# Optimization experiments

Hardware: AMD Instinct MI355X
Metric: run time of the kernel (lower is better)

Reference implementation:

```python
import jax, jax.numpy as jnp
import numpy as np

HIDDEN = 1024
HEADS = 16
HEAD_DIM = HIDDEN // HEADS


def setup_inputs() -> dict:
    key = jax.random.key(0)
    ks = jax.random.split(key, 7)
    B, S, H = 8, 1024, HIDDEN
    hidden_states = jax.random.normal(ks[0], (B, S, H), dtype=jnp.float32)
    attention_mask = jnp.zeros((B, 1, 1, S), dtype=jnp.float32)
    # Xavier-uniform weights [out, in], zero biases (matches module init)
    limit = float(np.sqrt(6.0 / (H + H)))
    Wq = jax.random.uniform(ks[1], (H, H), minval=-limit, maxval=limit, dtype=jnp.float32)
    Wk = jax.random.uniform(ks[2], (H, H), minval=-limit, maxval=limit, dtype=jnp.float32)
    Wv = jax.random.uniform(ks[3], (H, H), minval=-limit, maxval=limit, dtype=jnp.float32)
    bq = jnp.zeros((H,), dtype=jnp.float32)
    bk = jnp.zeros((H,), dtype=jnp.float32)
    bv = jnp.zeros((H,), dtype=jnp.float32)
    return {"hidden_states": hidden_states, "attention_mask": attention_mask,
            "Wq": Wq, "bq": bq, "Wk": Wk, "bk": bk, "Wv": Wv, "bv": bv}


def _split_heads(x):
    # [B, S, H] -> [B, heads, S, head_dim]
    B, S, _ = x.shape
    return x.reshape(B, S, HEADS, HEAD_DIM).transpose(0, 2, 1, 3)


def reference(hidden_states, attention_mask, Wq, bq, Wk, bk, Wv, bv):
    # Linear projections: y = x @ W^T + b  (weights stored [out, in] as in torch)
    q = _split_heads(hidden_states @ Wq.T + bq)
    k = _split_heads(hidden_states @ Wk.T + bk)
    v = _split_heads(hidden_states @ Wv.T + bv)
    scale = 1.0 / (HEAD_DIM ** 0.5)
    scores = jnp.einsum('bhqd,bhkd->bhqk', q, k) * scale  # [B,heads,S,S]
    scores = scores + attention_mask
    probs = jax.nn.softmax(scores, axis=-1)
    # dropout is identity at inference
    ctx = jnp.einsum('bhqk,bhkd->bhqd', probs, v)
    B, _, S, _ = ctx.shape
    return ctx.transpose(0, 2, 1, 3).reshape(B, S, HIDDEN)
```

## Files before the change

### kernel.cpp

```cpp
#include <hip/hip_runtime.h>
#include <hip/hip_bf16.h>
#include <stdint.h>

#define B_ 8
#define S_ 1024
#define NH_ 16
#define D_ 64
#define H_ 1024
#define M_TOT (B_*S_)
#define LOG2E 1.44269504088896f

typedef __attribute__((ext_vector_type(8))) short short8;
typedef __attribute__((ext_vector_type(4))) float f32x4;
typedef __attribute__((ext_vector_type(16))) float f32x16;

#if __has_builtin(__builtin_amdgcn_exp2f)
#define EXP2(x) __builtin_amdgcn_exp2f(x)
#else
#define EXP2(x) __expf((x) * 0.69314718056f)
#endif

static __device__ __forceinline__ unsigned short f2bf(float f) {
  union { float f; unsigned u; } c; c.f = f;
  unsigned u = c.u;
  return (unsigned short)((u + 0x7fffu + ((u >> 16) & 1u)) >> 16);
}

static __device__ __forceinline__ void gld_lds16(void* lds, const void* g) {
  __builtin_amdgcn_global_load_lds((const __attribute__((address_space(1))) unsigned*)g,
                                   (__attribute__((address_space(3))) unsigned*)lds, 16, 0, 0);
}

#define WAIT_LGKM0() asm volatile("s_waitcnt lgkmcnt(0)" ::: "memory")
#define WAIT_VM(n)   asm volatile("s_waitcnt vmcnt(" #n ")" ::: "memory")
#define SBAR()       __builtin_amdgcn_s_barrier()
#define SCHED0()     __builtin_amdgcn_sched_barrier(0)
#define PRIO1()      __builtin_amdgcn_s_setprio(1)
#define PRIO0()      __builtin_amdgcn_s_setprio(0)

__global__ void cvt_f32_bf16(const float* __restrict__ X,
                             const float* __restrict__ Wq,
                             const float* __restrict__ Wk,
                             const float* __restrict__ Wv,
                             unsigned short* __restrict__ Xbf,
                             unsigned short* __restrict__ Wbf) {
  const long long NX = (long long)M_TOT * H_;
  const long long NW = (long long)H_ * H_;
  long long t = (long long)blockIdx.x * blockDim.x + threadIdx.x;
  const long long stride = (long long)gridDim.x * blockDim.x;
  const long long total4 = (NX + 3 * NW) >> 2;
  for (; t < total4; t += stride) {
    long long e = t << 2;
    const float* src; unsigned short* dst;
    if (e < NX) { src = X + e; dst = Xbf + e; }
    else {
      long long r = e - NX;
      int w = (int)(r / NW);
      long long o = r - (long long)w * NW;
      src = (w == 0 ? Wq : (w == 1 ? Wk : Wv)) + o;
      dst = Wbf + (long long)w * NW + o;
    }
    float4 v = *(const float4*)src;
    ushort4 u;
    u.x = f2bf(v.x); u.y = f2bf(v.y); u.z = f2bf(v.z); u.w = f2bf(v.w);
    *(ushort4*)dst = u;
  }
}

#define QBM 256
#define QBN 256
#define QBK 64
#define REG_B 32768
#define BUFSZ 65536
#define VBUF  49152

#define MMQ(I0, J0, AF, BF)                                               \
  _Pragma("unroll")                                                       \
  for (int a_ = 0; a_ < 4; ++a_)                                          \
    _Pragma("unroll")                                                     \
    for (int b_ = 0; b_ < 2; ++b_)                                        \
      _Pragma("unroll")                                                   \
      for (int k_ = 0; k_ < 2; ++k_)                                      \
        acc[(I0) + a_][(J0) + b_] = __builtin_amdgcn_mfma_f32_16x16x32_bf16( \
            AF[a_][k_], BF[b_][k_], acc[(I0) + a_][(J0) + b_], 0, 0, 0);

#define RD_A(BUF, MS)                                                     \
  _Pragma("unroll")                                                       \
  for (int f_ = 0; f_ < 4; ++f_)                                          \
    _Pragma("unroll")                                                     \
    for (int k_ = 0; k_ < 2; ++k_) A[f_][k_] = rdA(BUF, MS, f_, k_);

#define RD_B(DST, BUF, NS)                                                \
  _Pragma("unroll")                                                       \
  for (int f_ = 0; f_ < 2; ++f_)                                          \
    _Pragma("unroll")                                                     \
    for (int k_ = 0; k_ < 2; ++k_) DST[f_][k_] = rdB(BUF, NS, f_, k_);

__global__ __launch_bounds__(512, 1) void qkv_gemm_qk(
    const unsigned short* __restrict__ Xbf,
    const unsigned short* __restrict__ Wbf,
    const float* __restrict__ bq, const float* __restrict__ bk,
    unsigned short* __restrict__ Qo, unsigned short* __restrict__ Ko) {
  __shared__ char lds[2 * BUFSZ];

  const int tid = threadIdx.x;
  const int w = tid >> 6;
  const int l = tid & 63;
  const int lrow = l & 15, lgrp = l >> 4;
  const int wm = w >> 2, wn = w & 3;

  const int orig = blockIdx.x;
  const int xcd = orig & 7;
  const int slot = orig >> 3;
  const int nz = slot >> 2;
  const int mtile = (xcd * 4 + (slot & 3)) * QBM;
  const int ntile = (nz & 3) * QBN;
  const int z = nz >> 2;

  const unsigned short* Wz = Wbf + (long long)z * H_ * H_;

  const int srow = l >> 3;
  const int sslot = l & 7;
  auto stageOpA = [&](char* buf, int half, int k0) {
    #pragma unroll
    for (int jj = 0; jj < 2; ++jj) {
      int j = w * 2 + jj;
      int row = half * 128 + j * 8 + srow;
      int so = (sslot ^ (row & 7)) * 8;
      gld_lds16(buf + (half * 16 + j) * 1024,
                Xbf + (long long)(mtile + row) * H_ + k0 + so);
    }
  };
  auto stageOpB = [&](char* buf, int half, int k0) {
    #pragma unroll
    for (int jj = 0; jj < 2; ++jj) {
      int j = w * 2 + jj;
      int row = half * 128 + j * 8 + srow;
      int so = (sslot ^ (row & 7)) * 8;
      gld_lds16(buf + REG_B + (half * 16 + j) * 1024,
                Wz + (long long)(ntile + row) * H_ + k0 + so);
    }
  };

  auto rdA = [&](const char* buf, int ms, int fi, int ks) -> short8 {
    int r = ms * 128 + wm * 64 + fi * 16 + lrow;
    return *(const short8*)(buf + r * 128 + (((ks * 4 + lgrp) ^ (r & 7)) * 16));
  };
  auto rdB = [&](const char* buf, int ns, int fj, int ks) -> short8 {
    int r = ns * 128 + wn * 32 + fj * 16 + lrow;
    return *(const short8*)(buf + REG_B + r * 128 + (((ks * 4 + lgrp) ^ (r & 7)) * 16));
  };

  f32x4 acc[8][4];
  f32x4 zero = {0.f, 0.f, 0.f, 0.f};
  #pragma unroll
  for (int a = 0; a < 8; ++a)
    #pragma unroll
    for (int c = 0; c < 4; ++c) acc[a][c] = zero;

  short8 A[4][2], B0[2][2], B1[2][2];

  stageOpA(lds, 0, 0);
  stageOpB(lds, 0, 0);
  stageOpB(lds, 1, 0);
  stageOpA(lds, 1, 0);
  stageOpA(lds + BUFSZ, 0, QBK);
  SCHED0(); WAIT_VM(6); SCHED0();
  SBAR();

  #pragma unroll 1
  for (int t = 0; t < 15; ++t) {
    char* bc = lds + ((t & 1) ? BUFSZ : 0);
    char* bn = lds + ((t & 1) ? 0 : BUFSZ);
    const int k1 = (t + 1) * QBK;
    const int k2 = (t + 2) * QBK;
    const bool st2 = (t + 2 < 16);

    RD_A(bc, 0);
    RD_B(B0, bc, 0);
    stageOpB(bn, 0, k1);
    WAIT_LGKM0(); SCHED0();
    PRIO1(); MMQ(0, 0, A, B0); PRIO0();
    SCHED0(); WAIT_VM(6); SCHED0();
    SBAR();

    RD_B(B1, bc, 1);
    stageOpB(bn, 1, k1);
    WAIT_LGKM0(); SCHED0();
    PRIO1(); MMQ(0, 2, A, B1); PRIO0();
    SCHED0(); WAIT_VM(6); SCHED0();
    SBAR();

    RD_A(bc, 1);
    stageOpA(bn, 1, k1);
    WAIT_LGKM0(); SCHED0();
    PRIO1(); MMQ(4, 2, A, B1); PRIO0();
    SCHED0(); WAIT_VM(6); SCHED0();
    SBAR();

    if (st2) stageOpA(bc, 0, k2);
    PRIO1(); MMQ(4, 0, A, B0); PRIO0();
    SCHED0(); WAIT_VM(6); SCHED0();
    SBAR();
  }

  SCHED0(); WAIT_VM(0); SCHED0();
  SBAR();
  {
    char* bc = lds + BUFSZ;
    RD_A(bc, 0);
    RD_B(B0, bc, 0);
    WAIT_LGKM0(); SCHED0();
    PRIO1(); MMQ(0, 0, A, B0); PRIO0();
    RD_B(B1, bc, 1);
    WAIT_LGKM0(); SCHED0();
    PRIO1(); MMQ(0, 2, A, B1); PRIO0();
    RD_A(bc, 1);
    WAIT_LGKM0(); SCHED0();
    PRIO1(); MMQ(4, 2, A, B1); MMQ(4, 0, A, B0); PRIO0();
  }

  const float* bias = (z == 0) ? bq : bk;
  unsigned short* O = (z == 0) ? Qo : Ko;
  #pragma unroll
  for (int nj = 0; nj < 4; ++nj) {
    int n = ntile + (nj >> 1) * 128 + wn * 32 + (nj & 1) * 16 + lrow;
    float bv_ = bias[n];
    int h = n >> 6, d = n & 63;
    #pragma unroll
    for (int mi = 0; mi < 8; ++mi)
      #pragma unroll
      for (int r = 0; r < 4; ++r) {
        int m = mtile + (mi >> 2) * 128 + wm * 64 + (mi & 3) * 16 + lgrp * 4 + r;
        float val = acc[mi][nj][r] + bv_;
        if (z == 0) val *= 0.125f * LOG2E;
        int b = m >> 10, s = m & 1023;
        O[(((long long)(b * NH_ + h)) * S_ + s) * D_ + d] = f2bf(val);
      }
  }
}

__global__ __launch_bounds__(512, 1) void qkv_gemm_v(
    const unsigned short* __restrict__ Xbf,
    const unsigned short* __restrict__ Wbf,
    const float* __restrict__ bv,
    unsigned short* __restrict__ Vt) {
  __shared__ char lds[3 * VBUF];

  const int tid = threadIdx.x;
  const int w = tid >> 6;
  const int l = tid & 63;
  const int lrow = l & 15, lgrp = l >> 4;
  const int wm = w >> 2, wn = w & 3;

  const int orig = blockIdx.x;
  const int xcd = orig & 7;
  const int slot = orig >> 3;
  const int mtile = (xcd * 8 + (slot & 7)) * 128;
  const int ntile = (slot >> 3) * QBN;

  const unsigned short* Wz = Wbf + 2LL * H_ * H_;

  const int srow = l >> 3;
  const int sslot = l & 7;
  auto stageW = [&](char* buf, int half, int k0) {
    #pragma unroll
    for (int jj = 0; jj < 2; ++jj) {
      int j = w * 2 + jj;
      int row = half * 128 + j * 8 + srow;
      int so = (sslot ^ (row & 7)) * 8;
      gld_lds16(buf + (half * 16 + j) * 1024,
                Wz + (long long)(ntile + row) * H_ + k0 + so);
    }
  };
  auto stageX = [&](char* buf, int k0) {
    #pragma unroll
    for (int jj = 0; jj < 2; ++jj) {
      int j = w * 2 + jj;
      int row = j * 8 + srow;
      int so = (sslot ^ (row & 7)) * 8;
      gld_lds16(buf + 32768 + j * 1024,
                Xbf + (long long)(mtile + row) * H_ + k0 + so);
    }
  };

  auto rdA = [&](const char* buf, int ms, int fi, int ks) -> short8 {
    int r = ms * 128 + wm * 64 + fi * 16 + lrow;
    return *(const short8*)(buf + r * 128 + (((ks * 4 + lgrp) ^ (r & 7)) * 16));
  };
  auto rdB = [&](const char* buf, int ns, int fj, int ks) -> short8 {
    int r = wn * 32 + fj * 16 + lrow;
    (void)ns;
    return *(const short8*)(buf + 32768 + r * 128 + (((ks * 4 + lgrp) ^ (r & 7)) * 16));
  };

  f32x4 acc[8][2];
  f32x4 zero = {0.f, 0.f, 0.f, 0.f};
  #pragma unroll
  for (int a = 0; a < 8; ++a)
    #pragma unroll
    for (int c = 0; c < 2; ++c) acc[a][c] = zero;

  short8 A[4][2], B0[2][2];

  stageW(lds, 0, 0); stageW(lds, 1, 0); stageX(lds, 0);
  stageW(lds + VBUF, 0, QBK); stageW(lds + VBUF, 1, QBK); stageX(lds + VBUF, QBK);
  SCHED0(); WAIT_VM(6); SCHED0();
  SBAR();

  #pragma unroll 1
  for (int t = 0; t < 16; ++t) {
    char* bc = lds + (t % 3) * VBUF;
    char* b2 = lds + ((t + 2) % 3) * VBUF;
    const int k2 = (t + 2) * QBK;
    const bool st2 = (t + 2 < 16);

    RD_A(bc, 0);
    RD_B(B0, bc, 0);
    if (st2) { stageW(b2, 0, k2); stageW(b2, 1, k2); }
    WAIT_LGKM0(); SCHED0();
    PRIO1(); MMQ(0, 0, A, B0); PRIO0();
    SCHED0(); WAIT_VM(6); SCHED0();
    SBAR();

    RD_A(bc, 1);
    if (st2) stageX(b2, k2);
    WAIT_LGKM0(); SCHED0();
    PRIO1(); MMQ(4, 0, A, B0); PRIO0();
    SCHED0();
    if (t < 14) { WAIT_VM(6); } else { WAIT_VM(0); }
    SCHED0();
    SBAR();
  }

  #pragma unroll
  for (int mi = 0; mi < 8; ++mi)
    #pragma unroll
    for (int r = 0; r < 4; ++r) {
      int nfull = ntile + (mi >> 2) * 128 + wm * 64 + (mi & 3) * 16 + lgrp * 4 + r;
      float bv_ = bv[nfull];
      int h = nfull >> 6, d = nfull & 63;
      #pragma unroll
      for (int nj = 0; nj < 2; ++nj) {
        int mfull = mtile + wn * 32 + nj * 16 + lrow;
        float val = acc[mi][nj][r] + bv_;
        int b = mfull >> 10, s = mfull & 1023;
        Vt[(((long long)(b * NH_ + h)) * D_ + d) * S_ + s] = f2bf(val);
      }
    }
}

__global__ __launch_bounds__(256, 2) void attn_fused(
    const unsigned short* __restrict__ Qbf,
    const unsigned short* __restrict__ Kbf,
    const unsigned short* __restrict__ Vtb,
    const float* __restrict__ mask,
    float* __restrict__ out) {
  __shared__ char lds[2 * 16384 + 4096];
  char* ldsM = lds + 32768;
  const int tid = threadIdx.x, w = tid >> 6, l = tid & 63;
  const int l31 = l & 31, h = l >> 5;

  const int lid = blockIdx.x;
  const int xcd = lid & 7, k = lid >> 3;
  const int bh = xcd * 16 + (k >> 3);
  const int qt = k & 7;
  const int b = bh >> 4, hd = bh & 15;
  const int q0 = qt * 128 + w * 32;

  const unsigned short* Kg = Kbf + (long long)bh * S_ * D_;
  const unsigned short* Vg = Vtb + (long long)bh * D_ * S_;
  const float* mrow = mask + b * S_;

  auto stageKV = [&](int kt, char* buf) {
    const int key0 = kt * 64;
    #pragma unroll
    for (int t = 0; t < 2; ++t) {
      int j = w * 2 + t;
      int row = j * 8 + (l >> 3);
      int so = ((l & 7) ^ (row & 7)) * 8;
      gld_lds16(buf + j * 1024,        Kg + (long long)(key0 + row) * D_ + so);
      gld_lds16(buf + 8192 + j * 1024, Vg + (long long)row * S_ + key0 + so);
    }
  };

  short8 qf[4];
  #pragma unroll
  for (int ks = 0; ks < 4; ++ks)
    qf[ks] = *(const short8*)(Qbf + ((long long)bh * S_ + q0 + l31) * D_ + ks * 16 + 8 * h);
  {
    float4 mv = *(const float4*)(mrow + tid * 4);
    f32x4 mt;
    mt[0] = mv.x * LOG2E - 12.f;
    mt[1] = mv.y * LOG2E - 12.f;
    mt[2] = mv.z * LOG2E - 12.f;
    mt[3] = mv.w * LOG2E - 12.f;
    *(f32x4*)(ldsM + tid * 16) = mt;
  }
  stageKV(0, lds);
  SCHED0(); WAIT_VM(0); SCHED0();
  __syncthreads();

  f32x16 acc[2];
  #pragma unroll
  for (int db = 0; db < 2; ++db)
    #pragma unroll
    for (int r = 0; r < 16; ++r) acc[db][r] = 0.f;
  float l_run = 0.f;

  #pragma unroll 1
  for (int kt = 0; kt < S_ / 64; ++kt) {
    char* ldsK = lds + (kt & 1) * 16384;
    char* ldsV = ldsK + 8192;
    const int key0 = kt * 64;
    const bool st = (kt + 1 < S_ / 64);

    if (st) stageKV(kt + 1, lds + ((kt + 1) & 1) * 16384);

    f32x16 sc[2];
    #pragma unroll
    for (int kb = 0; kb < 2; ++kb)
      #pragma unroll
      for (int r = 0; r < 16; ++r) sc[kb][r] = 0.f;

    #pragma unroll
    for (int kb = 0; kb < 2; ++kb) {
      short8 kf[4];
      #pragma unroll
      for (int ks = 0; ks < 4; ++ks) {
        int row = kb * 32 + l31;
        int g = (2 * ks + h) ^ (row & 7);
        kf[ks] = *(const short8*)(ldsK + row * 128 + g * 16);
      }
      PRIO1();
      #pragma unroll
      for (int ks = 0; ks < 4; ++ks)
        sc[kb] = __builtin_amdgcn_mfma_f32_32x32x16_bf16(
            kf[ks], qf[ks], sc[kb], 0, 0, 0);
      PRIO0();
    }

    float sv[32];
    #pragma unroll
    for (int kb = 0; kb < 2; ++kb)
      #pragma unroll
      for (int rg = 0; rg < 4; ++rg) {
        f32x4 m4 = *(const f32x4*)(ldsM + (key0 + kb * 32 + rg * 8 + 4 * h) * 4);
        #pragma unroll
        for (int c = 0; c < 4; ++c)
          sv[kb * 16 + rg * 4 + c] = EXP2(sc[kb][rg * 4 + c] + m4[c]);
      }
    {
      float r16[16];
      #pragma unroll
      for (int i = 0; i < 16; ++i) r16[i] = sv[i] + sv[i + 16];
      #pragma unroll
      for (int i = 0; i < 8; ++i) r16[i] = r16[i] + r16[i + 8];
      #pragma unroll
      for (int i = 0; i < 4; ++i) r16[i] = r16[i] + r16[i + 4];
      float ps = (r16[0] + r16[1]) + (r16[2] + r16[3]);
      float xs = ps, ys = ps;
      asm volatile("v_permlane32_swap_b32 %0, %1" : "+v"(xs), "+v"(ys));
      l_run += xs + ys;
    }

    short8 pfrag[4];
    {
      unsigned Wd[8][2];
      #pragma unroll
      for (int j = 0; j < 8; ++j) {
        int base = (j >> 2) * 16 + (j & 3) * 4;
        asm("v_cvt_pk_bf16_f32 %0, %1, %2" : "=v"(Wd[j][0]) : "v"(sv[base + 0]), "v"(sv[base + 1]));
        asm("v_cvt_pk_bf16_f32 %0, %1, %2" : "=v"(Wd[j][1]) : "v"(sv[base + 2]), "v"(sv[base + 3]));
      }
      #pragma unroll
      for (int ks = 0; ks < 4; ++ks) {
        unsigned x0 = Wd[2 * ks][0], y0 = Wd[2 * ks + 1][0];
        unsigned x1 = Wd[2 * ks][1], y1 = Wd[2 * ks + 1][1];
        asm volatile("v_permlane32_swap_b32 %0, %1" : "+v"(x0), "+v"(y0));
        asm volatile("v_permlane32_swap_b32 %0, %1" : "+v"(x1), "+v"(y1));
        union { unsigned u[4]; short8 s; } fu;
        fu.u[0] = x0;
        fu.u[1] = x1;
        fu.u[2] = y0;
        fu.u[3] = y1;
        pfrag[ks] = fu.s;
      }
    }

    #pragma unroll
    for (int db = 0; db < 2; ++db) {
      short8 vf[4];
      #pragma unroll
      for (int ks = 0; ks < 4; ++ks) {
        int row = db * 32 + l31;
        int g = (2 * ks + h) ^ (row & 7);
        vf[ks] = *(const short8*)(ldsV + row * 128 + g * 16);
      }
      PRIO1();
      #pragma unroll
      for (int ks = 0; ks < 4; ++ks)
        acc[db] = __builtin_amdgcn_mfma_f32_32x32x16_bf16(
            vf[ks], pfrag[ks], acc[db], 0, 0, 0);
      PRIO0();
    }

    if (st) { SCHED0(); WAIT_VM(0); SCHED0(); SBAR(); }
  }

  {
    float inv = 1.0f / l_run;
    int q = q0 + l31;
    float* orow = out + ((long long)b * S_ + q) * H_ + hd * D_;
    #pragma unroll
    for (int db = 0; db < 2; ++db)
      #pragma unroll
      for (int rg = 0; rg < 4; ++rg) {
        f32x4 v4;
        #pragma unroll
        for (int c = 0; c < 4; ++c) v4[c] = acc[db][rg * 4 + c] * inv;
        *(f32x4*)(orow + db * 32 + rg * 8 + 4 * h) = v4;
      }
  }
}

extern "C" void kernel_launch(void* const* d_in, const int* in_sizes, int n_in,
                              void* d_out, int out_size, void* d_ws, size_t ws_size,
                              hipStream_t stream) {
  const float* X    = (const float*)d_in[0];
  const float* mask = (const float*)d_in[1];
  const float* Wq   = (const float*)d_in[2];
  const float* bq   = (const float*)d_in[3];
  const float* Wk   = (const float*)d_in[4];
  const float* bk   = (const float*)d_in[5];
  const float* Wv   = (const float*)d_in[6];
  const float* bv   = (const float*)d_in[7];
  float* out = (float*)d_out;

  char* ws = (char*)d_ws;
  unsigned short* Xbf = (unsigned short*)ws;
  unsigned short* Wbf = (unsigned short*)(ws + 16777216);
  unsigned short* Qb  = (unsigned short*)(ws + 23068672);
  unsigned short* Kb  = (unsigned short*)(ws + 39845888);
  unsigned short* Vt  = (unsigned short*)(ws + 56623104);

  hipLaunchKernelGGL(cvt_f32_bf16, dim3(2048), dim3(256), 0, stream,
                     X, Wq, Wk, Wv, Xbf, Wbf);
  hipLaunchKernelGGL(qkv_gemm_qk, dim3(256), dim3(512), 0, stream,
                     Xbf, Wbf, bq, bk, Qb, Kb);
  hipLaunchKernelGGL(qkv_gemm_v, dim3(256), dim3(512), 0, stream,
                     Xbf, Wbf, bv, Vt);
  hipLaunchKernelGGL(attn_fused, dim3(1024), dim3(256), 0, stream,
                     Qb, Kb, Vt, mask, out);
}
```

Baseline: 117.1 us.

## Software-pipeline QK^T one tile ahead of softmax and PV in attention

Restructures the attention key loop so the QK^T MFMA for tile t+1 is issued before the exp/softmax and PV work of tile t, using ping-pong score registers (scA/scB) and a two-iteration unrolled loop. K and V staging are split: K is prefetched two tiles ahead and V one tile ahead, each with its own double buffer. The goal is to overlap matrix-core work with the exp and conversion VALU work and hide load latency. This costs extra VGPRs for the second score buffer, which could hurt occupancy at launch bounds (256,2), and relies on the barrier placement being correct for the new buffer reuse distances.

```diff
diff --git a/kernel.cpp b/kernel.cpp
--- a/kernel.cpp
+++ b/kernel.cpp
@@ -350,13 +350,108 @@
     }
 }
 
+#define ATTN_QK(DST, KBUF)                                                 \
+  {                                                                        \
+    _Pragma("unroll")                                                      \
+    for (int kb_ = 0; kb_ < 2; ++kb_) {                                    \
+      short8 kf[4];                                                        \
+      _Pragma("unroll")                                                    \
+      for (int ks_ = 0; ks_ < 4; ++ks_) {                                  \
+        int row_ = kb_ * 32 + l31;                                         \
+        int g_ = (2 * ks_ + h) ^ (row_ & 7);                               \
+        kf[ks_] = *(const short8*)((KBUF) + row_ * 128 + g_ * 16);         \
+      }                                                                    \
+      _Pragma("unroll")                                                    \
+      for (int r_ = 0; r_ < 16; ++r_) DST[kb_][r_] = 0.f;                  \
+      PRIO1();                                                             \
+      _Pragma("unroll")                                                    \
+      for (int ks_ = 0; ks_ < 4; ++ks_)                                    \
+        DST[kb_] = __builtin_amdgcn_mfma_f32_32x32x16_bf16(                \
+            kf[ks_], qf[ks_], DST[kb_], 0, 0, 0);                          \
+      PRIO0();                                                             \
+    }                                                                      \
+  }
+
+#define ATTN_BODY(T, CUR, NXT)                                             \
+  {                                                                        \
+    const int t_ = (T);                                                    \
+    const bool hasN = (t_ + 1 < 16);                                       \
+    if (t_ + 2 < 16) stageK(t_ + 2, lds + ((t_ & 1) << 13));               \
+    if (hasN) stageV(t_ + 1, lds + 16384 + (((t_ + 1) & 1) << 13));        \
+    if (hasN) { ATTN_QK(NXT, lds + (((t_ + 1) & 1) << 13)); }              \
+    const int key0_ = t_ * 64;                                             \
+    _Pragma("unroll")                                                      \
+    for (int kb_ = 0; kb_ < 2; ++kb_)                                      \
+      _Pragma("unroll")                                                    \
+      for (int rg_ = 0; rg_ < 4; ++rg_) {                                  \
+        f32x4 m4 = *(const f32x4*)(ldsM + (key0_ + kb_ * 32 + rg_ * 8 + 4 * h) * 4); \
+        _Pragma("unroll")                                                  \
+        for (int c_ = 0; c_ < 4; ++c_)                                     \
+          CUR[kb_][rg_ * 4 + c_] = EXP2(CUR[kb_][rg_ * 4 + c_] + m4[c_]);  \
+      }                                                                    \
+    {                                                                      \
+      float r16[16];                                                       \
+      _Pragma("unroll")                                                    \
+      for (int i_ = 0; i_ < 16; ++i_) r16[i_] = CUR[0][i_] + CUR[1][i_];   \
+      _Pragma("unroll")                                                    \
+      for (int i_ = 0; i_ < 8; ++i_) r16[i_] = r16[i_] + r16[i_ + 8];      \
+      _Pragma("unroll")                                                    \
+      for (int i_ = 0; i_ < 4; ++i_) r16[i_] = r16[i_] + r16[i_ + 4];      \
+      float ps = (r16[0] + r16[1]) + (r16[2] + r16[3]);                    \
+      float xs = ps, ys = ps;                                              \
+      asm volatile("v_permlane32_swap_b32 %0, %1" : "+v"(xs), "+v"(ys));   \
+      l_run += xs + ys;                                                    \
+    }                                                                      \
+    short8 pfrag[4];                                                       \
+    {                                                                      \
+      unsigned Wd[8][2];                                                   \
+      _Pragma("unroll")                                                    \
+      for (int j_ = 0; j_ < 8; ++j_) {                                     \
+        asm("v_cvt_pk_bf16_f32 %0, %1, %2" : "=v"(Wd[j_][0])               \
+            : "v"(CUR[j_ >> 2][(j_ & 3) * 4 + 0]), "v"(CUR[j_ >> 2][(j_ & 3) * 4 + 1])); \
+        asm("v_cvt_pk_bf16_f32 %0, %1, %2" : "=v"(Wd[j_][1])               \
+            : "v"(CUR[j_ >> 2][(j_ & 3) * 4 + 2]), "v"(CUR[j_ >> 2][(j_ & 3) * 4 + 3])); \
+      }                                                                    \
+      _Pragma("unroll")                                                    \
+      for (int ks_ = 0; ks_ < 4; ++ks_) {                                  \
+        unsigned x0 = Wd[2 * ks_][0], y0 = Wd[2 * ks_ + 1][0];             \
+        unsigned x1 = Wd[2 * ks_][1], y1 = Wd[2 * ks_ + 1][1];             \
+        asm volatile("v_permlane32_swap_b32 %0, %1" : "+v"(x0), "+v"(y0)); \
+        asm volatile("v_permlane32_swap_b32 %0, %1" : "+v"(x1), "+v"(y1)); \
+        union { unsigned u[4]; short8 s; } fu;                             \
+        fu.u[0] = x0; fu.u[1] = x1; fu.u[2] = y0; fu.u[3] = y1;            \
+        pfrag[ks_] = fu.s;                                                 \
+      }                                                                    \
+    }                                                                      \
+    {                                                                      \
+      char* vb = lds + 16384 + ((t_ & 1) << 13);                           \
+      _Pragma("unroll")                                                    \
+      for (int db_ = 0; db_ < 2; ++db_) {                                  \
+        short8 vf[4];                                                      \
+        _Pragma("unroll")                                                  \
+        for (int ks_ = 0; ks_ < 4; ++ks_) {                                \
+          int row_ = db_ * 32 + l31;                                       \
+          int g_ = (2 * ks_ + h) ^ (row_ & 7);                             \
+          vf[ks_] = *(const short8*)(vb + row_ * 128 + g_ * 16);           \
+        }                                                                  \
+        PRIO1();                                                           \
+        _Pragma("unroll")                                                  \
+        for (int ks_ = 0; ks_ < 4; ++ks_)                                  \
+          acc[db_] = __builtin_amdgcn_mfma_f32_32x32x16_bf16(              \
+              vf[ks_], pfrag[ks_], acc[db_], 0, 0, 0);                     \
+        PRIO0();                                                           \
+      }                                                                    \
+    }                                                                      \
+    if (hasN) { SCHED0(); WAIT_VM(0); SCHED0(); SBAR(); }                  \
+  }
+
 __global__ __launch_bounds__(256, 2) void attn_fused(
     const unsigned short* __restrict__ Qbf,
     const unsigned short* __restrict__ Kbf,
     const unsigned short* __restrict__ Vtb,
     const float* __restrict__ mask,
     float* __restrict__ out) {
-  __shared__ char lds[2 * 16384 + 4096];
+  __shared__ char lds[2 * 8192 + 2 * 8192 + 4096];
   char* ldsM = lds + 32768;
   const int tid = threadIdx.x, w = tid >> 6, l = tid & 63;
   const int l31 = l & 31, h = l >> 5;
@@ -372,15 +467,24 @@
   const unsigned short* Vg = Vtb + (long long)bh * D_ * S_;
   const float* mrow = mask + b * S_;
 
-  auto stageKV = [&](int kt, char* buf) {
+  auto stageK = [&](int kt, char* buf) {
     const int key0 = kt * 64;
     #pragma unroll
     for (int t = 0; t < 2; ++t) {
       int j = w * 2 + t;
       int row = j * 8 + (l >> 3);
       int so = ((l & 7) ^ (row & 7)) * 8;
-      gld_lds16(buf + j * 1024,        Kg + (long long)(key0 + row) * D_ + so);
-      gld_lds16(buf + 8192 + j * 1024, Vg + (long long)row * S_ + key0 + so);
+      gld_lds16(buf + j * 1024, Kg + (long long)(key0 + row) * D_ + so);
+    }
+  };
+  auto stageV = [&](int kt, char* buf) {
+    const int key0 = kt * 64;
+    #pragma unroll
+    for (int t = 0; t < 2; ++t) {
+      int j = w * 2 + t;
+      int row = j * 8 + (l >> 3);
+      int so = ((l & 7) ^ (row & 7)) * 8;
+      gld_lds16(buf + j * 1024, Vg + (long long)row * S_ + key0 + so);
     }
   };
 
@@ -397,7 +501,9 @@
     mt[3] = mv.w * LOG2E - 12.f;
     *(f32x4*)(ldsM + tid * 16) = mt;
   }
-  stageKV(0, lds);
+  stageK(0, lds);
+  stageV(0, lds + 16384);
+  stageK(1, lds + 8192);
   SCHED0(); WAIT_VM(0); SCHED0();
   __syncthreads();
 
@@ -408,104 +514,15 @@
     for (int r = 0; r < 16; ++r) acc[db][r] = 0.f;
   float l_run = 0.f;
 
+  f32x16 scA[2], scB[2];
+  ATTN_QK(scA, lds);
+  WAIT_LGKM0(); SCHED0();
+  SBAR();
+
   #pragma unroll 1
-  for (int kt = 0; kt < S_ / 64; ++kt) {
-    char* ldsK = lds + (kt & 1) * 16384;
-    char* ldsV = ldsK + 8192;
-    const int key0 = kt * 64;
-    const bool st = (kt + 1 < S_ / 64);
-
-    if (st) stageKV(kt + 1, lds + ((kt + 1) & 1) * 16384);
-
-    f32x16 sc[2];
-    #pragma unroll
-    for (int kb = 0; kb < 2; ++kb)
-      #pragma unroll
-      for (int r = 0; r < 16; ++r) sc[kb][r] = 0.f;
-
-    #pragma unroll
-    for (int kb = 0; kb < 2; ++kb) {
-      short8 kf[4];
-      #pragma unroll
-      for (int ks = 0; ks < 4; ++ks) {
-        int row = kb * 32 + l31;
-        int g = (2 * ks + h) ^ (row & 7);
-        kf[ks] = *(const short8*)(ldsK + row * 128 + g * 16);
-      }
-      PRIO1();
-      #pragma unroll
-      for (int ks = 0; ks < 4; ++ks)
-        sc[kb] = __builtin_amdgcn_mfma_f32_32x32x16_bf16(
-            kf[ks], qf[ks], sc[kb], 0, 0, 0);
-      PRIO0();
-    }
-
-    float sv[32];
-    #pragma unroll
-    for (int kb = 0; kb < 2; ++kb)
-      #pragma unroll
-      for (int rg = 0; rg < 4; ++rg) {
-        f32x4 m4 = *(const f32x4*)(ldsM + (key0 + kb * 32 + rg * 8 + 4 * h) * 4);
-        #pragma unroll
-        for (int c = 0; c < 4; ++c)
-          sv[kb * 16 + rg * 4 + c] = EXP2(sc[kb][rg * 4 + c] + m4[c]);
-      }
-    {
-      float r16[16];
-      #pragma unroll
-      for (int i = 0; i < 16; ++i) r16[i] = sv[i] + sv[i + 16];
-      #pragma unroll
-      for (int i = 0; i < 8; ++i) r16[i] = r16[i] + r16[i + 8];
-      #pragma unroll
-      for (int i = 0; i < 4; ++i) r16[i] = r16[i] + r16[i + 4];
-      float ps = (r16[0] + r16[1]) + (r16[2] + r16[3]);
-      float xs = ps, ys = ps;
-      asm volatile("v_permlane32_swap_b32 %0, %1" : "+v"(xs), "+v"(ys));
-      l_run += xs + ys;
-    }
-
-    short8 pfrag[4];
-    {
-      unsigned Wd[8][2];
-      #pragma unroll
-      for (int j = 0; j < 8; ++j) {
-        int base = (j >> 2) * 16 + (j & 3) * 4;
-        asm("v_cvt_pk_bf16_f32 %0, %1, %2" : "=v"(Wd[j][0]) : "v"(sv[base + 0]), "v"(sv[base + 1]));
-        asm("v_cvt_pk_bf16_f32 %0, %1, %2" : "=v"(Wd[j][1]) : "v"(sv[base + 2]), "v"(sv[base + 3]));
-      }
-      #pragma unroll
-      for (int ks = 0; ks < 4; ++ks) {
-        unsigned x0 = Wd[2 * ks][0], y0 = Wd[2 * ks + 1][0];
-        unsigned x1 = Wd[2 * ks][1], y1 = Wd[2 * ks + 1][1];
-        asm volatile("v_permlane32_swap_b32 %0, %1" : "+v"(x0), "+v"(y0));
-        asm volatile("v_permlane32_swap_b32 %0, %1" : "+v"(x1), "+v"(y1));
-        union { unsigned u[4]; short8 s; } fu;
-        fu.u[0] = x0;
-        fu.u[1] = x1;
-        fu.u[2] = y0;
-        fu.u[3] = y1;
-        pfrag[ks] = fu.s;
-      }
-    }
-
-    #pragma unroll
-    for (int db = 0; db < 2; ++db) {
-      short8 vf[4];
-      #pragma unroll
-      for (int ks = 0; ks < 4; ++ks) {
-        int row = db * 32 + l31;
-        int g = (2 * ks + h) ^ (row & 7);
-        vf[ks] = *(const short8*)(ldsV + row * 128 + g * 16);
-      }
-      PRIO1();
-      #pragma unroll
-      for (int ks = 0; ks < 4; ++ks)
-        acc[db] = __builtin_amdgcn_mfma_f32_32x32x16_bf16(
-            vf[ks], pfrag[ks], acc[db], 0, 0, 0);
-      PRIO0();
-    }
-
-    if (st) { SCHED0(); WAIT_VM(0); SCHED0(); SBAR(); }
+  for (int t = 0; t < 16; t += 2) {
+    ATTN_BODY(t,     scA, scB);
+    ATTN_BODY(t + 1, scB, scA);
   }
 
   {
```

Measured after the change: 120.2 us. 1.03x slower.
